# Kernel tuning notes

Hardware: AMD Instinct MI355X
Metric: run time of the kernel (lower is better)

Reference implementation:

```python
import jax, jax.numpy as jnp
import numpy as np

B = 4; E_PER = 100_000; E = B * E_PER
N_NODES = 50_000; N_REL = 500; D = 64; D_LG = 256
K_PER_VI = 20; S_VI = E // K_PER_VI          # 20000 sorted vi segments
S_VJ_PER = 5_000; S_VJ = B * S_VJ_PER        # 20000 unsorted vj segments
N_MEM = 131_072
INTERACT = ((0, 3), (0, 2, 3), (0, 4), (0, 2, 4), (1, 3), (1, 2, 3), (1, 4), (1, 2, 4))


def _build_edges():
    rng = np.random.default_rng(0)
    idx_vi = np.repeat(np.arange(S_VI), K_PER_VI)          # sorted segment ids
    gpb = S_VI // B
    eg = idx_vi // gpb                                     # sorted by eg_idx too
    vi = rng.integers(0, N_NODES, S_VI)[idx_vi]
    idx_vj = np.empty(E, dtype=np.int64)
    for b in range(B):
        loc = np.concatenate([np.arange(S_VJ_PER), rng.integers(0, S_VJ_PER, E_PER - S_VJ_PER)])
        rng.shuffle(loc)
        idx_vj[b * E_PER:(b + 1) * E_PER] = b * S_VJ_PER + loc  # every group non-empty
    vj = rng.integers(0, N_NODES, S_VJ)[idx_vj]            # consistent (eg, vj) per group
    rel = rng.integers(0, N_REL, E)
    e2vi = rng.integers(0, N_MEM, E)
    e2vj = rng.integers(0, N_MEM, E)
    return np.stack([eg, vi, vj, rel, idx_vi, idx_vj, e2vi, e2vj], axis=1).astype(np.int32)


def setup_inputs() -> dict:
    key = jax.random.key(0)
    ks = jax.random.split(key, 10)
    return {
        "node_attention": jax.random.uniform(ks[0], (B, N_NODES), jnp.float32),
        "scanned_edges": jnp.asarray(_build_edges()),
        "edges_y": jax.random.uniform(ks[1], (E,), jnp.float32),
        "hidden_uncon": jax.random.normal(ks[2], (1, N_NODES, D_LG), jnp.float32),
        "hidden_con": jax.random.normal(ks[3], (N_MEM, D), jnp.float32),
        "Wc": jax.random.normal(ks[4], (D, D), jnp.float32) / np.sqrt(D).astype(np.float32),
        "bc": jnp.zeros((D,), jnp.float32),
        "Wu": jax.random.normal(ks[5], (D_LG, D), jnp.float32) / np.sqrt(D_LG).astype(np.float32),
        "bu": jnp.zeros((D,), jnp.float32),
        "rel_table": jax.random.normal(ks[6], (N_REL, D), jnp.float32) * 0.05,
        "ws": jax.random.normal(ks[7], (len(INTERACT), D), jnp.float32) / np.sqrt(float(len(INTERACT))).astype(np.float32) if False else jax.random.normal(ks[7], (len(INTERACT), D), jnp.float32) * (1.0 / np.sqrt(len(INTERACT)).astype(np.float32)),
        "fb": jnp.zeros((D,), jnp.float32),
        "out_w": jax.random.normal(ks[8], (D,), jnp.float32),
        "out_b": jnp.zeros((D,), jnp.float32),
        "n_vi_segments": S_VI,
        "n_vj_segments": S_VJ,
    }


def reference(node_attention, scanned_edges, edges_y, hidden_uncon, hidden_con,
              Wc, bc, Wu, bu, rel_table, ws, fb, out_w, out_b,
              n_vi_segments, n_vj_segments):
    eg, vi, vj, rel = (scanned_edges[:, i] for i in range(4))
    idx_vi, idx_vj, e2vi, e2vj = (scanned_edges[:, i] for i in range(4, 8))
    # projections (proj_con / proj_uncon, tanh Dense)
    hc = jnp.tanh(hidden_con @ Wc + bc)          # [N_MEM, D]
    hu = jnp.tanh(hidden_uncon @ Wu + bu)[0]     # [n_nodes, D]; batch_size==1 path of Node2Edge
    # Node2Edge gathers
    feats = (hc[e2vi], hu[vi], rel_table[rel], hc[e2vj], hu[vj])  # each [E, D]
    # F layer: weighted sum of elementwise interaction products
    out = fb
    for k, idxs in enumerate(INTERACT):
        x = feats[idxs[0]]
        for i in idxs[1:]:
            x = x * feats[i]
        out = out + x * ws[k]
    out = jax.nn.relu(out) * out_w + out_b
    logits = jnp.sum(out, axis=1)                # [E]
    # NeighborSoftmax at 'vi' (sorted segment softmax)
    m = jax.ops.segment_max(logits, idx_vi, num_segments=n_vi_segments)
    ex = jnp.exp(logits - m[idx_vi])
    den = jax.ops.segment_sum(ex, idx_vi, num_segments=n_vi_segments)
    transition = ex / den[idx_vi]
    # attention flow: gather source attention, weight, aggregate at vj
    trans_att = transition * node_attention[eg, vi] * edges_y
    aggr = jax.ops.segment_sum(trans_att, idx_vj, num_segments=n_vj_segments)
    b_g = jax.ops.segment_max(eg, idx_vj, num_segments=n_vj_segments)
    vj_g = jax.ops.segment_max(vj, idx_vj, num_segments=n_vj_segments)
    new_node_attention = jnp.zeros_like(node_attention).at[b_g, vj_g].add(aggr)
    return new_node_attention
```

## Files before the change

kernel.cpp:

```cpp
#include <hip/hip_runtime.h>
#include <hip/hip_bf16.h>

#define D 64
#define KPER 20

typedef __attribute__((ext_vector_type(8))) short short8;
typedef __attribute__((ext_vector_type(4))) float floatx4;

__device__ __forceinline__ short f2bf(float x) {
    __hip_bfloat16 h = __float2bfloat16(x);
    return *reinterpret_cast<short*>(&h);
}

template<typename T> __device__ __forceinline__ T to_T(float x);
template<> __device__ __forceinline__ float to_T<float>(float x) { return x; }
template<> __device__ __forceinline__ __hip_bfloat16 to_T<__hip_bfloat16>(float x) { return __float2bfloat16(x); }

template<typename T> __device__ __forceinline__ float to_f(T x);
template<> __device__ __forceinline__ float to_f<float>(float x) { return x; }
template<> __device__ __forceinline__ float to_f<__hip_bfloat16>(__hip_bfloat16 x) { return __bfloat162float(x); }

__device__ __forceinline__ float fast_tanh(float x) {
    float xc = fminf(fmaxf(x, -15.f), 15.f);
    float e = __expf(2.f * xc);
    return 1.f - 2.f * __builtin_amdgcn_rcpf(1.f + e);
}

template<int CTRL>
__device__ __forceinline__ float dpp_add(float x) {
    int t = __builtin_amdgcn_update_dpp(0, __float_as_int(x), CTRL, 0xf, 0xf, true);
    return x + __int_as_float(t);
}
template<int CTRL>
__device__ __forceinline__ float dpp_max(float x) {
    int xi = __float_as_int(x);
    int t = __builtin_amdgcn_update_dpp(xi, xi, CTRL, 0xf, 0xf, false);
    return fmaxf(x, __int_as_float(t));
}
__device__ __forceinline__ float wave_sum_b(float x) {
    x = dpp_add<0x111>(x); x = dpp_add<0x112>(x);
    x = dpp_add<0x114>(x); x = dpp_add<0x118>(x);
    x = dpp_add<0x142>(x); x = dpp_add<0x143>(x);
    return __int_as_float(__builtin_amdgcn_readlane(__float_as_int(x), 63));
}
__device__ __forceinline__ float wave_max_b(float x) {
    x = dpp_max<0x111>(x); x = dpp_max<0x112>(x);
    x = dpp_max<0x114>(x); x = dpp_max<0x118>(x);
    x = dpp_max<0x142>(x); x = dpp_max<0x143>(x);
    return __int_as_float(__builtin_amdgcn_readlane(__float_as_int(x), 63));
}

template<int K, int CTN, typename T>
__device__ __forceinline__ void proj_body(const float* __restrict__ h,
        const float* __restrict__ W, const float* __restrict__ b,
        T* __restrict__ out, int ct0, int rt0, int rtstride, int ntiles) {
    constexpr int KT = K / 32;
    int lane = threadIdx.x & 63;
    int m = lane & 15, quad = lane >> 4;
    short8 bfr[CTN][KT];
    #pragma unroll
    for (int ct = 0; ct < CTN; ++ct)
        #pragma unroll
        for (int kt = 0; kt < KT; ++kt)
            #pragma unroll
            for (int j = 0; j < 8; ++j)
                bfr[ct][kt][j] = f2bf(W[(size_t)(kt * 32 + quad * 8 + j) * 64 + (ct0 + ct) * 16 + m]);
    float bv[CTN];
    #pragma unroll
    for (int ct = 0; ct < CTN; ++ct) bv[ct] = b[(ct0 + ct) * 16 + m];
    for (int rt = rt0; rt < ntiles; rt += rtstride) {
        floatx4 acc[CTN];
        #pragma unroll
        for (int ct = 0; ct < CTN; ++ct) acc[ct] = floatx4{0.f, 0.f, 0.f, 0.f};
        const float* hrow = h + (size_t)(rt * 16 + m) * K + quad * 8;
        #pragma unroll
        for (int kt = 0; kt < KT; ++kt) {
            floatx4 a0 = *(const floatx4*)(hrow + kt * 32);
            floatx4 a1 = *(const floatx4*)(hrow + kt * 32 + 4);
            short8 af;
            af[0] = f2bf(a0[0]); af[1] = f2bf(a0[1]);
            af[2] = f2bf(a0[2]); af[3] = f2bf(a0[3]);
            af[4] = f2bf(a1[0]); af[5] = f2bf(a1[1]);
            af[6] = f2bf(a1[2]); af[7] = f2bf(a1[3]);
            #pragma unroll
            for (int ct = 0; ct < CTN; ++ct)
                acc[ct] = __builtin_amdgcn_mfma_f32_16x16x32_bf16(af, bfr[ct][kt], acc[ct], 0, 0, 0);
        }
        #pragma unroll
        for (int ct = 0; ct < CTN; ++ct) {
            int col = (ct0 + ct) * 16 + m;
            #pragma unroll
            for (int reg = 0; reg < 4; ++reg) {
                int row = rt * 16 + quad * 4 + reg;
                out[(size_t)row * 64 + col] = to_T<T>(fast_tanh(acc[ct][reg] + bv[ct]));
            }
        }
    }
}

template<typename T>
__global__ __launch_bounds__(256) void proj_fused(
        const float* __restrict__ hcon, const float* __restrict__ Wc, const float* __restrict__ bc,
        const float* __restrict__ hun, const float* __restrict__ Wu, const float* __restrict__ bu,
        T* __restrict__ hc, T* __restrict__ hu, int t64, int t256, int g64) {
    int w = threadIdx.x >> 6;
    if ((int)blockIdx.x < g64) {
        int wid = blockIdx.x * 4 + w;
        proj_body<64, 4, T>(hcon, Wc, bc, hc, 0, wid, g64 * 4, t64);
    } else {
        int g256 = gridDim.x - g64;
        int wid = (blockIdx.x - g64) * 4 + w;
        int half = wid & 1;
        proj_body<256, 2, T>(hun, Wu, bu, hu, half * 2, wid >> 1, (g256 * 4) >> 1, t256);
    }
}

template<typename T>
__global__ __launch_bounds__(256) void edge_kernel(
        const float* __restrict__ natt, const int* __restrict__ edges,
        const float* __restrict__ ey, const T* __restrict__ hc,
        const T* __restrict__ hu, const float* __restrict__ relt,
        const float* __restrict__ wsm, const float* __restrict__ fb,
        const float* __restrict__ outw, float* __restrict__ out, int N) {
    int lane = threadIdx.x & 63;
    int s = blockIdx.x * 4 + (threadIdx.x >> 6);
    long base = (long)s * KPER;
    const int* e0 = edges + base * 8;
    int eg = e0[0], vi = e0[1];
    float f1 = to_f<T>(hu[(size_t)vi * D + lane]);
    float na = natt[(size_t)eg * N + vi];
    float w0 = wsm[0 * D + lane], w1 = wsm[1 * D + lane];
    float w2 = wsm[2 * D + lane], w3 = wsm[3 * D + lane];
    float w4 = wsm[4 * D + lane], w5 = wsm[5 * D + lane];
    float w6 = wsm[6 * D + lane], w7 = wsm[7 * D + lane];
    float fbv = fb[lane], owv = outw[lane];
    float myl = -INFINITY;
    int myvj = 0;
    #pragma unroll 4
    for (int e = 0; e < KPER; ++e) {
        const int* er = edges + (base + e) * 8;
        int vj = er[2], rel = er[3], evi = er[6], evj = er[7];
        float F0 = to_f<T>(hc[(size_t)evi * D + lane]);
        float F2 = relt[(size_t)rel * D + lane];
        float F3 = to_f<T>(hc[(size_t)evj * D + lane]);
        float F4 = to_f<T>(hu[(size_t)vj * D + lane]);
        float t1 = fmaf(F2, w1, w0);
        float t2 = fmaf(F2, w5, w4);
        float t3 = fmaf(F2, w3, w2);
        float t4 = fmaf(F2, w7, w6);
        float u = fmaf(F0, t1, f1 * t2);
        float v = fmaf(F0, t3, f1 * t4);
        float o = fmaf(F3, u, fmaf(F4, v, fbv));
        o = fmaxf(o, 0.0f) * owv;
        float tot = wave_sum_b(o);
        bool mine = (lane == e);
        myl = mine ? tot : myl;
        myvj = mine ? vj : myvj;
    }
    float mx = wave_max_b(myl);
    float ex = __expf(myl - mx);
    float den = wave_sum_b(ex);
    if (lane < KPER) {
        float t = (ex / den) * na * ey[base + lane];
        atomicAdd(out + (size_t)eg * N + myvj, t);
    }
}

extern "C" void kernel_launch(void* const* d_in, const int* in_sizes, int n_in,
                              void* d_out, int out_size, void* d_ws, size_t ws_size,
                              hipStream_t stream) {
    const float* natt = (const float*)d_in[0];
    const int*   edges = (const int*)d_in[1];
    const float* ey   = (const float*)d_in[2];
    const float* hun  = (const float*)d_in[3];
    const float* hcon = (const float*)d_in[4];
    const float* Wc   = (const float*)d_in[5];
    const float* bc   = (const float*)d_in[6];
    const float* Wu   = (const float*)d_in[7];
    const float* bu   = (const float*)d_in[8];
    const float* relt = (const float*)d_in[9];
    const float* wsm  = (const float*)d_in[10];
    const float* fb   = (const float*)d_in[11];
    const float* outw = (const float*)d_in[12];
    float* out = (float*)d_out;

    int E    = in_sizes[2];
    int S    = E / KPER;
    int nmem = in_sizes[4] / D;
    int N    = in_sizes[3] / 256;

    hipMemsetAsync(d_out, 0, (size_t)out_size * sizeof(float), stream);

    int t64  = nmem / 16;
    int t256 = N / 16;
    int g64  = 512, g256 = 512;

    size_t need_f32 = ((size_t)nmem + (size_t)N) * D * sizeof(float);
    if (ws_size >= need_f32) {
        float* hc = (float*)d_ws;
        float* hu = hc + (size_t)nmem * D;
        proj_fused<float><<<g64 + g256, 256, 0, stream>>>(hcon, Wc, bc, hun, Wu, bu,
                                                          hc, hu, t64, t256, g64);
        edge_kernel<float><<<S / 4, 256, 0, stream>>>(natt, edges, ey, hc, hu,
                                                      relt, wsm, fb, outw, out, N);
    } else {
        __hip_bfloat16* hc = (__hip_bfloat16*)d_ws;
        __hip_bfloat16* hu = hc + (size_t)nmem * D;
        proj_fused<__hip_bfloat16><<<g64 + g256, 256, 0, stream>>>(hcon, Wc, bc, hun, Wu, bu,
                                                                   hc, hu, t64, t256, g64);
        edge_kernel<__hip_bfloat16><<<S / 4, 256, 0, stream>>>(natt, edges, ey, hc, hu,
                                                               relt, wsm, fb, outw, out, N);
    }
}
```

Measured before the change: 224.7 us.

## Always store projections and relation table in bf16, preload edge rows per wave

Removes the fp32 workspace path so the projected hc/hu tables are always bf16. The relation table is also converted to bf16 by extra blocks added to the projection kernel. The edge kernel now loads a segment's 20 edge records with one coalesced wave load and broadcasts the fields by readlane in a fully unrolled loop, instead of issuing scalar loads per edge. This roughly halves the bytes moved by the random gathers and shortens the dependent index-load chain. The cost is lower precision in the intermediates and more register pressure from the full unroll.

```diff
diff --git a/kernel.cpp b/kernel.cpp
--- a/kernel.cpp
+++ b/kernel.cpp
@@ -1,5 +1,6 @@
 #include <hip/hip_runtime.h>
 #include <hip/hip_bf16.h>
+#include <type_traits>
 
 #define D 64
 #define KPER 20
@@ -7,18 +8,13 @@
 typedef __attribute__((ext_vector_type(8))) short short8;
 typedef __attribute__((ext_vector_type(4))) float floatx4;
 
-__device__ __forceinline__ short f2bf(float x) {
+__device__ __forceinline__ unsigned short f2bfu(float x) {
     __hip_bfloat16 h = __float2bfloat16(x);
-    return *reinterpret_cast<short*>(&h);
-}
-
-template<typename T> __device__ __forceinline__ T to_T(float x);
-template<> __device__ __forceinline__ float to_T<float>(float x) { return x; }
-template<> __device__ __forceinline__ __hip_bfloat16 to_T<__hip_bfloat16>(float x) { return __float2bfloat16(x); }
-
-template<typename T> __device__ __forceinline__ float to_f(T x);
-template<> __device__ __forceinline__ float to_f<float>(float x) { return x; }
-template<> __device__ __forceinline__ float to_f<__hip_bfloat16>(__hip_bfloat16 x) { return __bfloat162float(x); }
+    return *reinterpret_cast<unsigned short*>(&h);
+}
+__device__ __forceinline__ float bfu2f(unsigned short u) {
+    return __uint_as_float(((unsigned)u) << 16);
+}
 
 __device__ __forceinline__ float fast_tanh(float x) {
     float xc = fminf(fmaxf(x, -15.f), 15.f);
@@ -50,10 +46,25 @@
     return __int_as_float(__builtin_amdgcn_readlane(__float_as_int(x), 63));
 }
 
-template<int K, int CTN, typename T>
+template<int I, int N, typename F>
+__device__ __forceinline__ void static_for(F&& f) {
+    if constexpr (I < N) {
+        f(std::integral_constant<int, I>{});
+        static_for<I + 1, N>(f);
+    }
+}
+
+template<int SLOT>
+__device__ __forceinline__ int get_slot(int m0, int m1, int m2) {
+    if constexpr (SLOT < 64)       return __builtin_amdgcn_readlane(m0, SLOT);
+    else if constexpr (SLOT < 128) return __builtin_amdgcn_readlane(m1, SLOT - 64);
+    else                           return __builtin_amdgcn_readlane(m2, SLOT - 128);
+}
+
+template<int K, int CTN>
 __device__ __forceinline__ void proj_body(const float* __restrict__ h,
         const float* __restrict__ W, const float* __restrict__ b,
-        T* __restrict__ out, int ct0, int rt0, int rtstride, int ntiles) {
+        unsigned short* __restrict__ out, int ct0, int rt0, int rtstride, int ntiles) {
     constexpr int KT = K / 32;
     int lane = threadIdx.x & 63;
     int m = lane & 15, quad = lane >> 4;
@@ -64,7 +75,7 @@
         for (int kt = 0; kt < KT; ++kt)
             #pragma unroll
             for (int j = 0; j < 8; ++j)
-                bfr[ct][kt][j] = f2bf(W[(size_t)(kt * 32 + quad * 8 + j) * 64 + (ct0 + ct) * 16 + m]);
+                bfr[ct][kt][j] = (short)f2bfu(W[(size_t)(kt * 32 + quad * 8 + j) * 64 + (ct0 + ct) * 16 + m]);
     float bv[CTN];
     #pragma unroll
     for (int ct = 0; ct < CTN; ++ct) bv[ct] = b[(ct0 + ct) * 16 + m];
@@ -78,10 +89,10 @@
             floatx4 a0 = *(const floatx4*)(hrow + kt * 32);
             floatx4 a1 = *(const floatx4*)(hrow + kt * 32 + 4);
             short8 af;
-            af[0] = f2bf(a0[0]); af[1] = f2bf(a0[1]);
-            af[2] = f2bf(a0[2]); af[3] = f2bf(a0[3]);
-            af[4] = f2bf(a1[0]); af[5] = f2bf(a1[1]);
-            af[6] = f2bf(a1[2]); af[7] = f2bf(a1[3]);
+            af[0] = (short)f2bfu(a0[0]); af[1] = (short)f2bfu(a0[1]);
+            af[2] = (short)f2bfu(a0[2]); af[3] = (short)f2bfu(a0[3]);
+            af[4] = (short)f2bfu(a1[0]); af[5] = (short)f2bfu(a1[1]);
+            af[6] = (short)f2bfu(a1[2]); af[7] = (short)f2bfu(a1[3]);
             #pragma unroll
             for (int ct = 0; ct < CTN; ++ct)
                 acc[ct] = __builtin_amdgcn_mfma_f32_16x16x32_bf16(af, bfr[ct][kt], acc[ct], 0, 0, 0);
@@ -92,42 +103,50 @@
             #pragma unroll
             for (int reg = 0; reg < 4; ++reg) {
                 int row = rt * 16 + quad * 4 + reg;
-                out[(size_t)row * 64 + col] = to_T<T>(fast_tanh(acc[ct][reg] + bv[ct]));
+                out[(size_t)row * 64 + col] = f2bfu(fast_tanh(acc[ct][reg] + bv[ct]));
             }
         }
     }
 }
 
-template<typename T>
+#define RELB 16
 __global__ __launch_bounds__(256) void proj_fused(
         const float* __restrict__ hcon, const float* __restrict__ Wc, const float* __restrict__ bc,
         const float* __restrict__ hun, const float* __restrict__ Wu, const float* __restrict__ bu,
-        T* __restrict__ hc, T* __restrict__ hu, int t64, int t256, int g64) {
+        const float* __restrict__ relf, unsigned short* __restrict__ hc,
+        unsigned short* __restrict__ hu, unsigned short* __restrict__ relb,
+        int t64, int t256, int g64, int g256, int nrel) {
+    int bid = blockIdx.x;
     int w = threadIdx.x >> 6;
-    if ((int)blockIdx.x < g64) {
-        int wid = blockIdx.x * 4 + w;
-        proj_body<64, 4, T>(hcon, Wc, bc, hc, 0, wid, g64 * 4, t64);
+    if (bid < g64) {
+        int wid = bid * 4 + w;
+        proj_body<64, 4>(hcon, Wc, bc, hc, 0, wid, g64 * 4, t64);
+    } else if (bid < g64 + g256) {
+        int wid = (bid - g64) * 4 + w;
+        int half = wid & 1;
+        proj_body<256, 2>(hun, Wu, bu, hu, half * 2, wid >> 1, (g256 * 4) >> 1, t256);
     } else {
-        int g256 = gridDim.x - g64;
-        int wid = (blockIdx.x - g64) * 4 + w;
-        int half = wid & 1;
-        proj_body<256, 2, T>(hun, Wu, bu, hu, half * 2, wid >> 1, (g256 * 4) >> 1, t256);
-    }
-}
-
-template<typename T>
+        int tid = (bid - g64 - g256) * 256 + threadIdx.x;
+        for (int i = tid; i < nrel; i += RELB * 256) relb[i] = f2bfu(relf[i]);
+    }
+}
+
 __global__ __launch_bounds__(256) void edge_kernel(
         const float* __restrict__ natt, const int* __restrict__ edges,
-        const float* __restrict__ ey, const T* __restrict__ hc,
-        const T* __restrict__ hu, const float* __restrict__ relt,
+        const float* __restrict__ ey, const unsigned short* __restrict__ hc,
+        const unsigned short* __restrict__ hu, const unsigned short* __restrict__ relt,
         const float* __restrict__ wsm, const float* __restrict__ fb,
         const float* __restrict__ outw, float* __restrict__ out, int N) {
     int lane = threadIdx.x & 63;
     int s = blockIdx.x * 4 + (threadIdx.x >> 6);
     long base = (long)s * KPER;
-    const int* e0 = edges + base * 8;
-    int eg = e0[0], vi = e0[1];
-    float f1 = to_f<T>(hu[(size_t)vi * D + lane]);
+    const int* eb = edges + base * 8;
+    int m0 = eb[lane];
+    int m1 = eb[64 + lane];
+    int m2 = (lane < 32) ? eb[128 + lane] : 0;
+    int eg = get_slot<0>(m0, m1, m2);
+    int vi = get_slot<1>(m0, m1, m2);
+    float f1 = bfu2f(hu[(size_t)vi * D + lane]);
     float na = natt[(size_t)eg * N + vi];
     float w0 = wsm[0 * D + lane], w1 = wsm[1 * D + lane];
     float w2 = wsm[2 * D + lane], w3 = wsm[3 * D + lane];
@@ -136,14 +155,16 @@
     float fbv = fb[lane], owv = outw[lane];
     float myl = -INFINITY;
     int myvj = 0;
-    #pragma unroll 4
-    for (int e = 0; e < KPER; ++e) {
-        const int* er = edges + (base + e) * 8;
-        int vj = er[2], rel = er[3], evi = er[6], evj = er[7];
-        float F0 = to_f<T>(hc[(size_t)evi * D + lane]);
-        float F2 = relt[(size_t)rel * D + lane];
-        float F3 = to_f<T>(hc[(size_t)evj * D + lane]);
-        float F4 = to_f<T>(hu[(size_t)vj * D + lane]);
+    static_for<0, KPER>([&](auto ec) {
+        constexpr int e = decltype(ec)::value;
+        int vj  = get_slot<e * 8 + 2>(m0, m1, m2);
+        int rel = get_slot<e * 8 + 3>(m0, m1, m2);
+        int evi = get_slot<e * 8 + 6>(m0, m1, m2);
+        int evj = get_slot<e * 8 + 7>(m0, m1, m2);
+        float F0 = bfu2f(hc[(size_t)evi * D + lane]);
+        float F2 = bfu2f(relt[(size_t)rel * D + lane]);
+        float F3 = bfu2f(hc[(size_t)evj * D + lane]);
+        float F4 = bfu2f(hu[(size_t)vj * D + lane]);
         float t1 = fmaf(F2, w1, w0);
         float t2 = fmaf(F2, w5, w4);
         float t3 = fmaf(F2, w3, w2);
@@ -156,7 +177,7 @@
         bool mine = (lane == e);
         myl = mine ? tot : myl;
         myvj = mine ? vj : myvj;
-    }
+    });
     float mx = wave_max_b(myl);
     float ex = __expf(myl - mx);
     float den = wave_sum_b(ex);
@@ -188,6 +209,7 @@
     int S    = E / KPER;
     int nmem = in_sizes[4] / D;
     int N    = in_sizes[3] / 256;
+    int nrel = in_sizes[9];
 
     hipMemsetAsync(d_out, 0, (size_t)out_size * sizeof(float), stream);
 
@@ -195,20 +217,13 @@
     int t256 = N / 16;
     int g64  = 512, g256 = 512;
 
-    size_t need_f32 = ((size_t)nmem + (size_t)N) * D * sizeof(float);
-    if (ws_size >= need_f32) {
-        float* hc = (float*)d_ws;
-        float* hu = hc + (size_t)nmem * D;
-        proj_fused<float><<<g64 + g256, 256, 0, stream>>>(hcon, Wc, bc, hun, Wu, bu,
-                                                          hc, hu, t64, t256, g64);
-        edge_kernel<float><<<S / 4, 256, 0, stream>>>(natt, edges, ey, hc, hu,
-                                                      relt, wsm, fb, outw, out, N);
-    } else {
-        __hip_bfloat16* hc = (__hip_bfloat16*)d_ws;
-        __hip_bfloat16* hu = hc + (size_t)nmem * D;
-        proj_fused<__hip_bfloat16><<<g64 + g256, 256, 0, stream>>>(hcon, Wc, bc, hun, Wu, bu,
-                                                                   hc, hu, t64, t256, g64);
-        edge_kernel<__hip_bfloat16><<<S / 4, 256, 0, stream>>>(natt, edges, ey, hc, hu,
-                                                               relt, wsm, fb, outw, out, N);
-    }
-}
+    unsigned short* hc = (unsigned short*)d_ws;
+    unsigned short* hu = hc + (size_t)nmem * D;
+    unsigned short* rb = hu + (size_t)N * D;
+
+    proj_fused<<<g64 + g256 + RELB, 256, 0, stream>>>(hcon, Wc, bc, hun, Wu, bu,
+                                                      relt, hc, hu, rb,
+                                                      t64, t256, g64, g256, nrel);
+    edge_kernel<<<S / 4, 256, 0, stream>>>(natt, edges, ey, hc, hu, rb,
+                                           wsm, fb, outw, out, N);
+}
```

New measurement: 207.2 us. 1.08x faster.
